# Performance work log

Measured on AMD Instinct MI355X. Metric: run time of the kernel, lower is better.

## Reference

```python
import jax, jax.numpy as jnp
import numpy as np
from jax import lax

B, T, D = 2, 2048, 1024
D_STATE, EXPAND, K = 64, 2, 3
INNER = D * EXPAND
FF_MULT, E, TOP_K = 4, 4, 2
HID = D * FF_MULT


def setup_inputs() -> dict:
    key = jax.random.key(0)
    ks = jax.random.split(key, 20)
    s = 0.02
    inp = {
        "x": jax.random.normal(ks[0], (B, T, D), jnp.float32),
        "norm1_w": jnp.ones((D,), jnp.float32),
        "norm2_w": jnp.ones((D,), jnp.float32),
        "in_proj_w": jax.random.normal(ks[1], (D, 2 * INNER), jnp.float32) * s,
        "in_proj_b": jnp.zeros((2 * INNER,), jnp.float32),
        "conv_w": jax.random.normal(ks[2], (INNER, 1, K), jnp.float32) * s,
        "conv_b": jnp.zeros((INNER,), jnp.float32),
        "dt_w": jax.random.normal(ks[3], (INNER, D_STATE), jnp.float32) * s,
        "dt_b": jnp.zeros((D_STATE,), jnp.float32),
        "bp_w": jax.random.normal(ks[4], (INNER, D_STATE), jnp.float32) * s,
        "bp_b": jnp.zeros((D_STATE,), jnp.float32),
        "cp_w": jax.random.normal(ks[5], (INNER, D_STATE), jnp.float32) * s,
        "cp_b": jnp.zeros((D_STATE,), jnp.float32),
        "s2i_w": jax.random.normal(ks[6], (D_STATE, INNER), jnp.float32) * s,
        "s2i_b": jnp.zeros((INNER,), jnp.float32),
        "D_param": jnp.ones((INNER,), jnp.float32),
        "out_w": jax.random.normal(ks[7], (INNER, D), jnp.float32) * s,
        "out_b": jnp.zeros((D,), jnp.float32),
        "gate_w": jax.random.normal(ks[8], (D, E), jnp.float32) * s,
        "gate_b": jnp.zeros((E,), jnp.float32),
        "e_w1": jax.random.normal(ks[9], (E, D, HID), jnp.float32) * s,
        "e_b1": jnp.zeros((E, HID), jnp.float32),
        "e_w2": jax.random.normal(ks[10], (E, HID, D), jnp.float32) * s,
        "e_b2": jnp.zeros((E, D), jnp.float32),
    }
    return inp


def _rmsnorm(x, w, eps=1e-6):
    nr = lax.rsqrt(jnp.mean(x * x, axis=-1, keepdims=True) + eps)
    return x * nr * w


def _layernorm(x, eps=1e-5):
    mu = jnp.mean(x, axis=-1, keepdims=True)
    var = jnp.mean((x - mu) ** 2, axis=-1, keepdims=True)
    return (x - mu) * lax.rsqrt(var + eps)


def _mixer(h, in_proj_w, in_proj_b, conv_w, conv_b, dt_w, dt_b, bp_w, bp_b,
           cp_w, cp_b, s2i_w, s2i_b, D_param, out_w, out_b):
    seq_len = h.shape[1]
    xz = h @ in_proj_w + in_proj_b                      # [B,T,2*inner]
    x_main, gate = jnp.split(xz, 2, axis=-1)
    # causal depthwise conv: pad both sides k-1 (torch padding), slice to T
    xc = jnp.swapaxes(x_main, 1, 2)                      # [B,inner,T]
    xc = lax.conv_general_dilated(
        xc, conv_w, window_strides=(1,), padding=[(K - 1, K - 1)],
        dimension_numbers=("NCH", "OIH", "NCH"), feature_group_count=INNER)
    xc = xc[..., :seq_len] + conv_b[None, :, None]
    x_main = jax.nn.silu(jnp.swapaxes(xc, 1, 2))         # [B,T,inner]

    dt = jax.nn.sigmoid(x_main @ dt_w + dt_b)            # [B,T,S]
    Bm = x_main @ bp_w + bp_b
    Cm = x_main @ cp_w + cp_b

    def step(state, inp):
        dt_t, b_t, c_t = inp
        state = (1.0 - dt_t) * state + dt_t * b_t
        return state, c_t * state

    init = jnp.zeros((h.shape[0], D_STATE), h.dtype)
    _, y = lax.scan(step, init, (jnp.swapaxes(dt, 0, 1),
                                 jnp.swapaxes(Bm, 0, 1),
                                 jnp.swapaxes(Cm, 0, 1)))
    y = jnp.swapaxes(y, 0, 1)                            # [B,T,S]
    y = _layernorm(y)
    y = y @ s2i_w + s2i_b
    y = y + D_param * x_main
    y = y * jax.nn.sigmoid(gate)
    return y @ out_w + out_b


def _moe(h, gate_w, gate_b, e_w1, e_b1, e_w2, e_b2):
    logits = h @ gate_w + gate_b                         # [B,T,E]
    top_vals, top_idx = lax.top_k(logits, TOP_K)
    top_probs = jax.nn.softmax(top_vals, axis=-1)
    # per-expert combine weight (0 if not selected), matches dense masking
    w_full = jnp.sum(jax.nn.one_hot(top_idx, E, dtype=h.dtype)
                     * top_probs[..., None], axis=-2)    # [B,T,E]
    hid = jax.nn.gelu(jnp.einsum("btd,edh->ebth", h, e_w1)
                      + e_b1[:, None, None, :], approximate=False)
    eo = jnp.einsum("ebth,ehd->ebtd", hid, e_w2) + e_b2[:, None, None, :]
    return jnp.einsum("ebtd,bte->btd", eo, w_full)


def reference(x, norm1_w, norm2_w, in_proj_w, in_proj_b, conv_w, conv_b,
              dt_w, dt_b, bp_w, bp_b, cp_w, cp_b, s2i_w, s2i_b, D_param,
              out_w, out_b, gate_w, gate_b, e_w1, e_b1, e_w2, e_b2):
    x = x + _mixer(_rmsnorm(x, norm1_w), in_proj_w, in_proj_b, conv_w, conv_b,
                   dt_w, dt_b, bp_w, bp_b, cp_w, cp_b, s2i_w, s2i_b,
                   D_param, out_w, out_b)
    x = x + _moe(_rmsnorm(x, norm2_w), gate_w, gate_b, e_w1, e_b1, e_w2, e_b2)
    return x
```

## Files before the change

### kernel.cpp

```cpp
#include <hip/hip_runtime.h>
#include <hip/hip_bf16.h>
#include <math.h>
#include <stdint.h>

#define T_ 2048
#define NTOK 4096
#define MB (1024 * 1024)

typedef unsigned short bf16_t;
typedef __attribute__((ext_vector_type(8))) short short8;
typedef __attribute__((ext_vector_type(4))) float f32x4;
typedef __attribute__((ext_vector_type(4))) unsigned short us4;

__device__ __forceinline__ bf16_t f2bf(float f) {
  unsigned u = __float_as_uint(f);
  u += 0x7fffu + ((u >> 16) & 1u);
  return (bf16_t)(u >> 16);
}
__device__ __forceinline__ float bf2f(bf16_t h) {
  return __uint_as_float(((unsigned)h) << 16);
}
__device__ __forceinline__ float sigm(float x) { return 1.f / (1.f + __expf(-x)); }

__device__ __forceinline__ void gload_lds16(const bf16_t* g, bf16_t* l) {
  __builtin_amdgcn_global_load_lds(
      (const __attribute__((address_space(1))) void*)g,
      (__attribute__((address_space(3))) void*)l, 16, 0, 0);
}

template <int MODE, int BN>
__global__ __launch_bounds__(256) void gemm_bt(
    const bf16_t* __restrict__ A, const bf16_t* __restrict__ BT,
    int M, int N, int K,
    float* __restrict__ outf, bf16_t* __restrict__ outb,
    const float* __restrict__ bias,
    const bf16_t* __restrict__ xb0, int xs0,
    const bf16_t* __restrict__ xb1, int xs1,
    const float* __restrict__ xf0, int xfs0,
    const float* __restrict__ d0,
    const float* __restrict__ scale4,
    float* __restrict__ outf2,
    const int* __restrict__ gidx,
    const int* __restrict__ cntp) {
  constexpr int NJ = BN / 32;
  __shared__ __align__(16) bf16_t As[2][128 * 32];
  __shared__ __align__(16) bf16_t Bs[2][BN * 32];
  const int tid = threadIdx.x;
  const int wave = tid >> 6;
  const int lane = tid & 63;

  long m0, n0;
  const bf16_t* Bb = BT;
  const float* biasp = bias;
  int eSel = 0;
  if constexpr (MODE == 7 || MODE == 8) {
    const int mt = blockIdx.y, nt = blockIdx.x;
    if (mt >= cntp[0]) return;
    eSel = cntp[1 + mt] & 3;
    m0 = (long)mt * 128;
    n0 = (long)nt * BN;
    Bb = BT + (long)eSel * N * K;
    biasp = bias + (long)eSel * N;
  } else {
    const int tn = gridDim.x, tm = gridDim.y;
    const int id = blockIdx.y * tn + blockIdx.x;
    const int xcd = id & 7;
    const int s = id >> 3;
    const int pm = tm >> 2;
    const int pn = tn >> 1;
    const int mt = (xcd & 3) * pm + (s % pm);
    const int nt = (xcd >> 2) * pn + (s / pm);
    m0 = (long)mt * 128;
    n0 = (long)nt * BN;
  }

  f32x4 acc[4][NJ];
#pragma unroll
  for (int i = 0; i < 4; ++i)
#pragma unroll
    for (int j = 0; j < NJ; ++j) acc[i][j] = f32x4{0.f, 0.f, 0.f, 0.f};

  const int rowL = tid >> 2;
  const int qL = tid & 3;
  const int ks = (qL ^ ((rowL >> 1) & 3)) * 8;
  long r0 = m0 + rowL, r1 = m0 + rowL + 64;
  if constexpr (MODE == 7) {
    int t0k = gidx[r0], t1k = gidx[r1];
    r0 = (t0k < 0) ? 0 : t0k;
    r1 = (t1k < 0) ? 0 : t1k;
  }
  const bf16_t* pA0 = A + r0 * (long)K + ks;
  const bf16_t* pA1 = A + r1 * (long)K + ks;
  const bf16_t* pB0 = Bb + (n0 + rowL) * (long)K + ks;
  const bf16_t* pB1 = Bb + (n0 + rowL + 64) * (long)K + ks;
  bf16_t* lA0 = As[0] + wave * 512;
  bf16_t* lB0 = Bs[0] + wave * 512;
  bf16_t* lA1 = As[1] + wave * 512;
  bf16_t* lB1 = Bs[1] + wave * 512;

  const int wm = (wave & 1) * 64;
  const int wn = (wave >> 1) * (BN / 2);
  const int lm = lane & 15;
  const int kq = ((lane >> 4) ^ ((lm >> 1) & 3)) * 8;

  for (int k0 = 0; k0 < K; k0 += 64) {
    gload_lds16(pA0 + k0, lA0);
    gload_lds16(pA1 + k0, lA0 + 2048);
    gload_lds16(pB0 + k0, lB0);
    if constexpr (BN == 128) gload_lds16(pB1 + k0, lB0 + 2048);
    gload_lds16(pA0 + k0 + 32, lA1);
    gload_lds16(pA1 + k0 + 32, lA1 + 2048);
    gload_lds16(pB0 + k0 + 32, lB1);
    if constexpr (BN == 128) gload_lds16(pB1 + k0 + 32, lB1 + 2048);
    __syncthreads();
#pragma unroll
    for (int h = 0; h < 2; ++h) {
      short8 af[4], bfr[NJ];
#pragma unroll
      for (int i = 0; i < 4; ++i)
        af[i] = *(const short8*)(As[h] + (wm + i * 16 + lm) * 32 + kq);
#pragma unroll
      for (int j = 0; j < NJ; ++j)
        bfr[j] = *(const short8*)(Bs[h] + (wn + j * 16 + lm) * 32 + kq);
#pragma unroll
      for (int i = 0; i < 4; ++i)
#pragma unroll
        for (int j = 0; j < NJ; ++j)
          acc[i][j] = __builtin_amdgcn_mfma_f32_16x16x32_bf16(af[i], bfr[j], acc[i][j], 0, 0, 0);
    }
    __syncthreads();
  }

  const int er = (lane >> 4) * 4;
  const int ec = lane & 15;
#pragma unroll
  for (int i = 0; i < 4; ++i) {
#pragma unroll
    for (int j = 0; j < NJ; ++j) {
#pragma unroll
      for (int r = 0; r < 4; ++r) {
        long row = m0 + wm + i * 16 + er + r;
        long col = n0 + wn + j * 16 + ec;
        float v = acc[i][j][r] + biasp[col];
        if constexpr (MODE == 0) {
          outf[row * N + col] = v;
        } else if constexpr (MODE == 5) {
          outb[row * N + col] = f2bf(v);
        } else if constexpr (MODE == 1) {
          float xm = bf2f(xb0[row * (long)xs0 + col]);
          float g = bf2f(xb1[row * (long)xs1 + col]);
          v = (v + d0[col] * xm) * sigm(g);
          outb[row * N + col] = f2bf(v);
        } else if constexpr (MODE == 2) {
          v += xf0[row * (long)xfs0 + col];
          outf[row * N + col] = v;
          outf2[row * N + col] = v;
        } else if constexpr (MODE == 7) {
          v = 0.5f * v * (1.f + erff(v * 0.70710678118654752f));
          outb[row * N + col] = f2bf(v);
        } else if constexpr (MODE == 8) {
          int t = gidx[row];
          if (t >= 0)
            unsafeAtomicAdd(outf + (long)t * N + col, scale4[t * 4 + eSel] * v);
        }
      }
    }
  }
}

__global__ __launch_bounds__(256) void tcast_k(const float* __restrict__ in,
                                               bf16_t* __restrict__ out, int R, int C) {
  __shared__ float tile[32][33];
  const int tx = threadIdx.x, ty = threadIdx.y;
  const long c0 = (long)blockIdx.x * 32, r0 = (long)blockIdx.y * 32;
#pragma unroll
  for (int i = 0; i < 4; ++i) {
    int r = ty + i * 8;
    tile[r][tx] = in[(r0 + r) * (long)C + c0 + tx];
  }
  __syncthreads();
#pragma unroll
  for (int i = 0; i < 4; ++i) {
    int r = ty + i * 8;
    out[(c0 + r) * (long)R + r0 + tx] = f2bf(tile[tx][r]);
  }
}

__global__ void dtbias_k(const float* __restrict__ dtb, const float* __restrict__ bpb,
                         const float* __restrict__ cpb, float* __restrict__ out) {
  int i = threadIdx.x;
  float v = 0.f;
  if (i < 64) v = dtb[i];
  else if (i < 128) v = bpb[i - 64];
  else if (i < 192) v = cpb[i - 128];
  out[i] = v;
}

__global__ __launch_bounds__(256) void rmsnorm_k(const float* __restrict__ x,
                                                 const float* __restrict__ w,
                                                 bf16_t* __restrict__ ob) {
  const long row = blockIdx.x;
  const int tid = threadIdx.x;
  const int wave = tid >> 6, lane = tid & 63;
  const float4 v = ((const float4*)(x + row * 1024))[tid];
  float ss = v.x * v.x + v.y * v.y + v.z * v.z + v.w * v.w;
#pragma unroll
  for (int off = 32; off > 0; off >>= 1) ss += __shfl_down(ss, off);
  __shared__ float sred[4];
  if (lane == 0) sred[wave] = ss;
  __syncthreads();
  float tot = sred[0] + sred[1] + sred[2] + sred[3];
  float nr = rsqrtf(tot * (1.f / 1024.f) + 1e-6f);
  const float4 wv = ((const float4*)w)[tid];
  us4 o;
  o.x = f2bf(v.x * nr * wv.x);
  o.y = f2bf(v.y * nr * wv.y);
  o.z = f2bf(v.z * nr * wv.z);
  o.w = f2bf(v.w * nr * wv.w);
  ((us4*)ob)[row * 256 + tid] = o;
}

__global__ __launch_bounds__(256) void conv_silu_k(const bf16_t* __restrict__ xz,
                                                   const float* __restrict__ cw,
                                                   const float* __restrict__ cb,
                                                   bf16_t* __restrict__ xs) {
  long idx = (long)blockIdx.x * 256 + threadIdx.x;
  int c = (int)(idx & 2047);
  long row = idx >> 11;
  int t = (int)(row & 2047);
  const bf16_t* p = xz + row * 4096 + c;
  float v = bf2f(p[0]) * cw[c * 3 + 2];
  if (t >= 1) v += bf2f(*(p - 4096)) * cw[c * 3 + 1];
  if (t >= 2) v += bf2f(*(p - 8192)) * cw[c * 3 + 0];
  v += cb[c];
  v = v * sigm(v);
  xs[idx] = f2bf(v);
}

__global__ __launch_bounds__(256) void scan_k(const float* __restrict__ dtbc,
                                              float* __restrict__ y) {
  const int bid = blockIdx.x;
  const int b = bid >> 6, s = bid & 63;
  const int tid = threadIdx.x;
  const float* base = dtbc + (long)b * T_ * 256;
  const int t0 = tid * 8;
  float A = 1.f, U = 0.f;
#pragma unroll
  for (int i = 0; i < 8; ++i) {
    const float* r = base + (long)(t0 + i) * 256;
    float dt = sigm(r[s]);
    float bv = r[64 + s];
    U = (1.f - dt) * U + dt * bv;
    A = (1.f - dt) * A;
  }
  __shared__ float sA[256], sU[256];
  sA[tid] = A; sU[tid] = U;
  __syncthreads();
  for (int off = 1; off < 256; off <<= 1) {
    float pA = 1.f, pU = 0.f;
    if (tid >= off) { pA = sA[tid - off]; pU = sU[tid - off]; }
    __syncthreads();
    U = A * pU + U;
    A = A * pA;
    sA[tid] = A; sU[tid] = U;
    __syncthreads();
  }
  float st = (tid == 0) ? 0.f : sU[tid - 1];
#pragma unroll
  for (int i = 0; i < 8; ++i) {
    const float* r = base + (long)(t0 + i) * 256;
    float dt = sigm(r[s]);
    float bv = r[64 + s];
    st = (1.f - dt) * st + dt * bv;
    y[((long)b * T_ + t0 + i) * 64 + s] = r[128 + s] * st;
  }
}

__global__ __launch_bounds__(256) void ln64_k(const float* __restrict__ y,
                                              bf16_t* __restrict__ yb) {
  const int tid = threadIdx.x;
  const int wave = tid >> 6, lane = tid & 63;
  const long row = (long)blockIdx.x * 4 + wave;
  float v = y[row * 64 + lane];
  float m = v;
#pragma unroll
  for (int off = 32; off > 0; off >>= 1) m += __shfl_xor(m, off);
  m *= (1.f / 64.f);
  float d = v - m;
  float var = d * d;
#pragma unroll
  for (int off = 32; off > 0; off >>= 1) var += __shfl_xor(var, off);
  var *= (1.f / 64.f);
  yb[row * 64 + lane] = f2bf(d * rsqrtf(var + 1e-5f));
}

__global__ __launch_bounds__(256) void gate_k(const float* __restrict__ x2,
                                              const float* __restrict__ nw,
                                              const float* __restrict__ gw,
                                              const float* __restrict__ gb,
                                              float* __restrict__ w4) {
  const int tid = threadIdx.x;
  const int wave = tid >> 6, lane = tid & 63;
  const long t = (long)blockIdx.x * 4 + wave;
  float a0 = 0, a1 = 0, a2 = 0, a3 = 0, ssq = 0;
#pragma unroll
  for (int i = 0; i < 16; ++i) {
    int d = lane + i * 64;
    float xv = x2[t * 1024 + d];
    ssq += xv * xv;
    float h = xv * nw[d];
    float4 w = ((const float4*)gw)[d];
    a0 += h * w.x; a1 += h * w.y; a2 += h * w.z; a3 += h * w.w;
  }
#pragma unroll
  for (int off = 32; off > 0; off >>= 1) {
    a0 += __shfl_xor(a0, off); a1 += __shfl_xor(a1, off);
    a2 += __shfl_xor(a2, off); a3 += __shfl_xor(a3, off);
    ssq += __shfl_xor(ssq, off);
  }
  if (lane == 0) {
    float nr = rsqrtf(ssq * (1.f / 1024.f) + 1e-6f);
    float lg[4] = {a0 * nr + gb[0], a1 * nr + gb[1], a2 * nr + gb[2], a3 * nr + gb[3]};
    int i0 = 0;
    for (int e = 1; e < 4; ++e)
      if (lg[e] > lg[i0]) i0 = e;
    int i1 = -1;
    for (int e = 0; e < 4; ++e) {
      if (e == i0) continue;
      if (i1 < 0 || lg[e] > lg[i1]) i1 = e;
    }
    float e1 = __expf(lg[i1] - lg[i0]);
    float p0 = 1.f / (1.f + e1), p1 = e1 / (1.f + e1);
    float o[4] = {0.f, 0.f, 0.f, 0.f};
    o[i0] = p0; o[i1] = p1;
    w4[t * 4 + 0] = o[0]; w4[t * 4 + 1] = o[1];
    w4[t * 4 + 2] = o[2]; w4[t * 4 + 3] = o[3];
  }
}

__global__ __launch_bounds__(256) void build2_k(const float* __restrict__ w4,
                                                int* __restrict__ cidx,
                                                int* __restrict__ meta) {
  __shared__ int ps[256];
  __shared__ int tbase_s;
  const int tid = threadIdx.x;
  if (tid == 0) tbase_s = 0;
  __syncthreads();
  for (int e = 0; e < 4; ++e) {
    const int base = tid * 16;
    unsigned char loc[16];
    int c = 0;
#pragma unroll
    for (int i = 0; i < 16; ++i)
      if (w4[(long)(base + i) * 4 + e] != 0.f) loc[c++] = (unsigned char)i;
    ps[tid] = c;
    __syncthreads();
    for (int off = 1; off < 256; off <<= 1) {
      int v = (tid >= off) ? ps[tid - off] : 0;
      __syncthreads();
      ps[tid] += v;
      __syncthreads();
    }
    const int total = ps[255];
    const int p = ps[tid] - c;
    const int tbase = tbase_s;
    const int rowbase = tbase * 128;
    for (int i = 0; i < c; ++i) cidx[rowbase + p + i] = base + (int)loc[i];
    const int tiles = (total + 127) >> 7;
    for (int j = total + tid; j < tiles * 128; j += 256) cidx[rowbase + j] = -1;
    for (int j = tid; j < tiles; j += 256) meta[1 + tbase + j] = e;
    __syncthreads();
    if (tid == 0) tbase_s = tbase + tiles;
    __syncthreads();
  }
  if (tid == 0) meta[0] = tbase_s;
}

extern "C" void kernel_launch(void* const* d_in, const int* in_sizes, int n_in,
                              void* d_out, int out_size, void* d_ws, size_t ws_size,
                              hipStream_t stream) {
  const float* x = (const float*)d_in[0];
  const float* n1w = (const float*)d_in[1];
  const float* n2w = (const float*)d_in[2];
  const float* inpw = (const float*)d_in[3];
  const float* inpb = (const float*)d_in[4];
  const float* convw = (const float*)d_in[5];
  const float* convb = (const float*)d_in[6];
  const float* dtw = (const float*)d_in[7];
  const float* dtb = (const float*)d_in[8];
  const float* bpw = (const float*)d_in[9];
  const float* bpb = (const float*)d_in[10];
  const float* cpw = (const float*)d_in[11];
  const float* cpb = (const float*)d_in[12];
  const float* s2iw = (const float*)d_in[13];
  const float* s2ib = (const float*)d_in[14];
  const float* Dp = (const float*)d_in[15];
  const float* outw = (const float*)d_in[16];
  const float* outb_ = (const float*)d_in[17];
  const float* gatew = (const float*)d_in[18];
  const float* gateb = (const float*)d_in[19];
  const float* ew1 = (const float*)d_in[20];
  const float* eb1 = (const float*)d_in[21];
  const float* ew2 = (const float*)d_in[22];
  const float* eb2 = (const float*)d_in[23];
  float* out = (float*)d_out;

  char* ws = (char*)d_ws;
  size_t off = 0;
  auto alloc = [&](size_t bytes) -> void* {
    void* p = (void*)(ws + off);
    off += (bytes + 255) & ~(size_t)255;
    return p;
  };

  float* biasdt = (float*)alloc(256 * 4);
  float* ybuf = (float*)alloc((size_t)NTOK * 64 * 4);
  bf16_t* ylnb = (bf16_t*)alloc((size_t)NTOK * 64 * 2);
  float* x2 = (float*)alloc((size_t)NTOK * 1024 * 4);
  bf16_t* h2b = (bf16_t*)alloc((size_t)NTOK * 1024 * 2);
  float* w4 = (float*)alloc((size_t)NTOK * 4 * 4);
  int* cidx = (int*)alloc((size_t)68 * 128 * 4);
  int* meta = (int*)alloc(128 * 4);

  const size_t REG_SZ = 64 * (size_t)MB + (size_t)8704 * 4096 * 2;
  char* reg = (char*)alloc(REG_SZ);
  bf16_t* xzb = (bf16_t*)reg;
  bf16_t* xsb = (bf16_t*)(reg + 32 * (size_t)MB);
  float* dtbc = (float*)(reg + 48 * (size_t)MB);
  bf16_t* zb = (bf16_t*)(reg + 52 * (size_t)MB);
  bf16_t* inpT = (bf16_t*)(reg + 64 * (size_t)MB);
  bf16_t* outT = (bf16_t*)(reg + 72 * (size_t)MB);
  bf16_t* h1b = (bf16_t*)(reg + 76 * (size_t)MB);
  bf16_t* wdtT = (bf16_t*)(reg + 84 * (size_t)MB);
  bf16_t* s2iT = (bf16_t*)(reg + 85 * (size_t)MB);
  bf16_t* w1T = (bf16_t*)reg;
  bf16_t* w2T = (bf16_t*)(reg + 32 * (size_t)MB);
  bf16_t* hidb = (bf16_t*)(reg + 64 * (size_t)MB);

  dim3 tb(32, 8);
  hipMemsetAsync(wdtT, 0, (size_t)256 * 2048 * 2, stream);
  dtbias_k<<<1, 256, 0, stream>>>(dtb, bpb, cpb, biasdt);
  tcast_k<<<dim3(128, 32), tb, 0, stream>>>(inpw, inpT, 1024, 4096);
  tcast_k<<<dim3(2, 64), tb, 0, stream>>>(dtw, wdtT, 2048, 64);
  tcast_k<<<dim3(2, 64), tb, 0, stream>>>(bpw, wdtT + (size_t)64 * 2048, 2048, 64);
  tcast_k<<<dim3(2, 64), tb, 0, stream>>>(cpw, wdtT + (size_t)128 * 2048, 2048, 64);
  tcast_k<<<dim3(64, 2), tb, 0, stream>>>(s2iw, s2iT, 64, 2048);
  tcast_k<<<dim3(32, 64), tb, 0, stream>>>(outw, outT, 2048, 1024);

  rmsnorm_k<<<NTOK, 256, 0, stream>>>(x, n1w, h1b);
  gemm_bt<5, 128><<<dim3(32, 32), 256, 0, stream>>>(h1b, inpT, NTOK, 4096, 1024,
      nullptr, xzb, inpb, nullptr, 0, nullptr, 0, nullptr, 0, nullptr, nullptr,
      nullptr, nullptr, nullptr);
  conv_silu_k<<<(NTOK * 2048) / 256, 256, 0, stream>>>(xzb, convw, convb, xsb);
  gemm_bt<0, 64><<<dim3(4, 32), 256, 0, stream>>>(xsb, wdtT, NTOK, 256, 2048,
      dtbc, nullptr, biasdt, nullptr, 0, nullptr, 0, nullptr, 0, nullptr, nullptr,
      nullptr, nullptr, nullptr);
  scan_k<<<128, 256, 0, stream>>>(dtbc, ybuf);
  ln64_k<<<NTOK / 4, 256, 0, stream>>>(ybuf, ylnb);
  gemm_bt<1, 128><<<dim3(16, 32), 256, 0, stream>>>(ylnb, s2iT, NTOK, 2048, 64,
      nullptr, zb, s2ib, xsb, 2048, xzb + 2048, 4096, nullptr, 0, Dp, nullptr,
      nullptr, nullptr, nullptr);
  gemm_bt<2, 64><<<dim3(16, 32), 256, 0, stream>>>(zb, outT, NTOK, 1024, 2048,
      x2, nullptr, outb_, nullptr, 0, nullptr, 0, x, 1024, nullptr, nullptr, out,
      nullptr, nullptr);

  for (int e = 0; e < 4; ++e) {
    tcast_k<<<dim3(128, 32), tb, 0, stream>>>(ew1 + (size_t)e * 1024 * 4096,
        w1T + (size_t)e * 4096 * 1024, 1024, 4096);
    tcast_k<<<dim3(32, 128), tb, 0, stream>>>(ew2 + (size_t)e * 4096 * 1024,
        w2T + (size_t)e * 1024 * 4096, 4096, 1024);
  }
  rmsnorm_k<<<NTOK, 256, 0, stream>>>(x2, n2w, h2b);
  gate_k<<<NTOK / 4, 256, 0, stream>>>(x2, n2w, gatew, gateb, w4);
  build2_k<<<1, 256, 0, stream>>>(w4, cidx, meta);
  gemm_bt<7, 128><<<dim3(32, 68), 256, 0, stream>>>(h2b, w1T, 8704, 4096, 1024,
      nullptr, hidb, eb1, nullptr, 0, nullptr, 0, nullptr, 0, nullptr, nullptr,
      nullptr, cidx, meta);
  gemm_bt<8, 64><<<dim3(16, 68), 256, 0, stream>>>(hidb, w2T, 8704, 1024, 4096,
      out, nullptr, eb2, nullptr, 0, nullptr, 0, nullptr, 0, nullptr, w4,
      nullptr, cidx, meta);
}
```

Measured before the change: 748.5 us.

## Pack routed MoE rows, swizzle expert GEMM tiles, batch weight casts

Result: faster. 723.5 us (-3.3%).

```diff
diff --git a/kernel.cpp b/kernel.cpp
--- a/kernel.cpp
+++ b/kernel.cpp
@@ -54,7 +54,14 @@
   const float* biasp = bias;
   int eSel = 0;
   if constexpr (MODE == 7 || MODE == 8) {
-    const int mt = blockIdx.y, nt = blockIdx.x;
+    const int tn = gridDim.x, tm = gridDim.y;
+    const int id = blockIdx.y * tn + blockIdx.x;
+    const int xcd = id & 7;
+    const int s = id >> 3;
+    const int pm = (tm + 3) >> 2;
+    const int pn = tn >> 1;
+    const int mt = (xcd & 3) * pm + s / pn;
+    const int nt = (xcd >> 2) * pn + s % pn;
     if (mt >= cntp[0]) return;
     eSel = cntp[1 + mt] & 3;
     m0 = (long)mt * 128;
@@ -83,14 +90,8 @@
   const int rowL = tid >> 2;
   const int qL = tid & 3;
   const int ks = (qL ^ ((rowL >> 1) & 3)) * 8;
-  long r0 = m0 + rowL, r1 = m0 + rowL + 64;
-  if constexpr (MODE == 7) {
-    int t0k = gidx[r0], t1k = gidx[r1];
-    r0 = (t0k < 0) ? 0 : t0k;
-    r1 = (t1k < 0) ? 0 : t1k;
-  }
-  const bf16_t* pA0 = A + r0 * (long)K + ks;
-  const bf16_t* pA1 = A + r1 * (long)K + ks;
+  const bf16_t* pA0 = A + (m0 + rowL) * (long)K + ks;
+  const bf16_t* pA1 = A + (m0 + rowL + 64) * (long)K + ks;
   const bf16_t* pB0 = Bb + (n0 + rowL) * (long)K + ks;
   const bf16_t* pB1 = Bb + (n0 + rowL + 64) * (long)K + ks;
   bf16_t* lA0 = As[0] + wave * 512;
@@ -169,10 +170,13 @@
 }
 
 __global__ __launch_bounds__(256) void tcast_k(const float* __restrict__ in,
-                                               bf16_t* __restrict__ out, int R, int C) {
+                                               bf16_t* __restrict__ out, int R, int C,
+                                               long inz, long outz) {
   __shared__ float tile[32][33];
   const int tx = threadIdx.x, ty = threadIdx.y;
   const long c0 = (long)blockIdx.x * 32, r0 = (long)blockIdx.y * 32;
+  in += (long)blockIdx.z * inz;
+  out += (long)blockIdx.z * outz;
 #pragma unroll
   for (int i = 0; i < 4; ++i) {
     int r = ty + i * 8;
@@ -374,6 +378,18 @@
     __syncthreads();
   }
   if (tid == 0) meta[0] = tbase_s;
+}
+
+__global__ __launch_bounds__(256) void packA_k(const bf16_t* __restrict__ h2b,
+                                               const int* __restrict__ cidx,
+                                               bf16_t* __restrict__ apack) {
+  long idx = (long)blockIdx.x * 256 + threadIdx.x;
+  long row = idx >> 7;
+  int ch = (int)(idx & 127);
+  int t = cidx[row];
+  float4 v = make_float4(0.f, 0.f, 0.f, 0.f);
+  if (t >= 0) v = ((const float4*)(h2b + (long)t * 1024))[ch];
+  ((float4*)(apack + row * 1024))[ch] = v;
 }
 
 extern "C" void kernel_launch(void* const* d_in, const int* in_sizes, int n_in,
@@ -421,6 +437,7 @@
   float* w4 = (float*)alloc((size_t)NTOK * 4 * 4);
   int* cidx = (int*)alloc((size_t)68 * 128 * 4);
   int* meta = (int*)alloc(128 * 4);
+  bf16_t* apack = (bf16_t*)ybuf;
 
   const size_t REG_SZ = 64 * (size_t)MB + (size_t)8704 * 4096 * 2;
   char* reg = (char*)alloc(REG_SZ);
@@ -438,14 +455,13 @@
   bf16_t* hidb = (bf16_t*)(reg + 64 * (size_t)MB);
 
   dim3 tb(32, 8);
-  hipMemsetAsync(wdtT, 0, (size_t)256 * 2048 * 2, stream);
   dtbias_k<<<1, 256, 0, stream>>>(dtb, bpb, cpb, biasdt);
-  tcast_k<<<dim3(128, 32), tb, 0, stream>>>(inpw, inpT, 1024, 4096);
-  tcast_k<<<dim3(2, 64), tb, 0, stream>>>(dtw, wdtT, 2048, 64);
-  tcast_k<<<dim3(2, 64), tb, 0, stream>>>(bpw, wdtT + (size_t)64 * 2048, 2048, 64);
-  tcast_k<<<dim3(2, 64), tb, 0, stream>>>(cpw, wdtT + (size_t)128 * 2048, 2048, 64);
-  tcast_k<<<dim3(64, 2), tb, 0, stream>>>(s2iw, s2iT, 64, 2048);
-  tcast_k<<<dim3(32, 64), tb, 0, stream>>>(outw, outT, 2048, 1024);
+  tcast_k<<<dim3(128, 32), tb, 0, stream>>>(inpw, inpT, 1024, 4096, 0, 0);
+  tcast_k<<<dim3(2, 64), tb, 0, stream>>>(dtw, wdtT, 2048, 64, 0, 0);
+  tcast_k<<<dim3(2, 64), tb, 0, stream>>>(bpw, wdtT + (size_t)64 * 2048, 2048, 64, 0, 0);
+  tcast_k<<<dim3(2, 64), tb, 0, stream>>>(cpw, wdtT + (size_t)128 * 2048, 2048, 64, 0, 0);
+  tcast_k<<<dim3(64, 2), tb, 0, stream>>>(s2iw, s2iT, 64, 2048, 0, 0);
+  tcast_k<<<dim3(32, 64), tb, 0, stream>>>(outw, outT, 2048, 1024, 0, 0);
 
   rmsnorm_k<<<NTOK, 256, 0, stream>>>(x, n1w, h1b);
   gemm_bt<5, 128><<<dim3(32, 32), 256, 0, stream>>>(h1b, inpT, NTOK, 4096, 1024,
@@ -464,16 +480,15 @@
       x2, nullptr, outb_, nullptr, 0, nullptr, 0, x, 1024, nullptr, nullptr, out,
       nullptr, nullptr);
 
-  for (int e = 0; e < 4; ++e) {
-    tcast_k<<<dim3(128, 32), tb, 0, stream>>>(ew1 + (size_t)e * 1024 * 4096,
-        w1T + (size_t)e * 4096 * 1024, 1024, 4096);
-    tcast_k<<<dim3(32, 128), tb, 0, stream>>>(ew2 + (size_t)e * 4096 * 1024,
-        w2T + (size_t)e * 1024 * 4096, 4096, 1024);
-  }
+  tcast_k<<<dim3(128, 32, 4), tb, 0, stream>>>(ew1, w1T, 1024, 4096,
+      (long)1024 * 4096, (long)4096 * 1024);
+  tcast_k<<<dim3(32, 128, 4), tb, 0, stream>>>(ew2, w2T, 4096, 1024,
+      (long)4096 * 1024, (long)1024 * 4096);
   rmsnorm_k<<<NTOK, 256, 0, stream>>>(x2, n2w, h2b);
   gate_k<<<NTOK / 4, 256, 0, stream>>>(x2, n2w, gatew, gateb, w4);
   build2_k<<<1, 256, 0, stream>>>(w4, cidx, meta);
-  gemm_bt<7, 128><<<dim3(32, 68), 256, 0, stream>>>(h2b, w1T, 8704, 4096, 1024,
+  packA_k<<<(8704 * 128) / 256, 256, 0, stream>>>(h2b, cidx, apack);
+  gemm_bt<7, 128><<<dim3(32, 68), 256, 0, stream>>>(apack, w1T, 8704, 4096, 1024,
       nullptr, hidb, eb1, nullptr, 0, nullptr, 0, nullptr, 0, nullptr, nullptr,
       nullptr, cidx, meta);
   gemm_bt<8, 64><<<dim3(16, 68), 256, 0, stream>>>(hidb, w2T, 8704, 1024, 4096,
```
